# Kernel tuning notes

Measured on AMD Instinct MI355X. Metric: run time of the kernel, lower is better.

The kernel has to match this reference:

```python
import jax, jax.numpy as jnp
import numpy as np

T, D = 2048, 1024      # tokens, hidden_size
FF = 512               # moe_intermediate_size
E, K = 16, 4           # num_experts, top_k
L = 3                  # conv_L_cache (short causal conv width)
EPS = 1e-5
SCALE = 1.0            # routed_scaling_factor


def setup_inputs() -> dict:
    key = jax.random.key(0)
    ks = jax.random.split(key, 10)
    s = lambda k, shape, sc: jax.random.normal(k, shape, jnp.float32) * sc
    return {
        "hidden_states": s(ks[0], (T, D), 1.0),
        "residual": s(ks[1], (T, D), 1.0),
        "op_norm_w": jnp.ones((D,), jnp.float32),
        "ffn_norm_w": jnp.ones((D,), jnp.float32),
        "in_proj_w": s(ks[2], (3 * D, D), 0.02),   # produces B, C, x
        "conv_w": s(ks[3], (D, L), 0.2),            # depthwise causal kernel
        "out_proj_w": s(ks[4], (D, D), 0.02),
        "gate_w": s(ks[5], (E, D), 0.02),
        "gate_bias": s(ks[6], (E,), 0.1),           # e_score_correction_bias
        "w1": s(ks[7], (E, 2 * FF, D), 0.02),       # per-expert gate+up
        "w2": s(ks[8], (E, D, FF), 0.02),           # per-expert down
    }


def _fused_add_rmsnorm(x, w, res):
    # vLLM RMSNorm(x, residual): x += residual; residual = x; out = rmsnorm(x)*w
    x = x + res
    res = x
    v = jnp.mean(x * x, axis=-1, keepdims=True)
    return x * jax.lax.rsqrt(v + EPS) * w, res


def reference(hidden_states, residual, op_norm_w, ffn_norm_w, in_proj_w,
              conv_w, out_proj_w, gate_w, gate_bias, w1, w2):
    h, residual = _fused_add_rmsnorm(hidden_states, op_norm_w, residual)

    # ---- ShortConv mixer: Bx = B*x, causal depthwise conv, gate by C ----
    bcx = h @ in_proj_w.T                         # [T, 3D]
    B, C, x = jnp.split(bcx, 3, axis=-1)
    Bx = B * x
    xp = jnp.pad(Bx, ((L - 1, 0), (0, 0)))        # causal left-pad
    shifts = jnp.stack([xp[k:k + T] for k in range(L)], axis=0)  # [L,T,D]
    conv = jnp.einsum('ltd,dl->td', shifts, conv_w)
    y = (C * conv) @ out_proj_w.T                 # [T, D]

    h, residual = _fused_add_rmsnorm(y, ffn_norm_w, residual)

    # ---- Sparse MoE: sigmoid scoring + bias-corrected top-k, renormalize ----
    logits = h.astype(jnp.float32) @ gate_w.T     # [T, E]
    scores = jax.nn.sigmoid(logits)
    choice = scores + gate_bias                   # selection uses biased scores
    _, topi = jax.lax.top_k(choice, K)            # [T, K]
    w = jnp.take_along_axis(scores, topi, axis=-1)  # weights from raw scores
    w = w / (jnp.sum(w, axis=-1, keepdims=True) + 1e-20)  # norm_topk_prob
    cw = jnp.sum(jax.nn.one_hot(topi, E, dtype=h.dtype) * w[..., None].astype(h.dtype), axis=1)  # [T, E]

    # dense dispatch (reference): all experts on all tokens, masked combine
    gu = jnp.einsum('td,efd->etf', h, w1)         # [E, T, 2FF]
    g, u = jnp.split(gu, 2, axis=-1)
    act = jax.nn.silu(g) * u                      # SiluAndMul
    ye = jnp.einsum('etf,edf->etd', act, w2)      # [E, T, D]
    out = jnp.einsum('te,etd->td', cw, ye) * SCALE
    return out, residual
```

## Files before the change

kernel.cpp:

```cpp
#include <hip/hip_runtime.h>
#include <hip/hip_bf16.h>

#define T_  2048
#define D_  1024
#define FF_ 512
#define E_  16
#define K_  4
#define L_  3
static constexpr float EPS = 1e-5f;

typedef __hip_bfloat16 bf16;
typedef __attribute__((ext_vector_type(8))) short bf16x8;
typedef __attribute__((ext_vector_type(4))) float f32x4;

__device__ __forceinline__ float b2f(bf16 x) { return __bfloat162float(x); }

__device__ __forceinline__ unsigned int pk2(float a, float b) {
    __hip_bfloat162 h = __float22bfloat162_rn(make_float2(a, b));
    unsigned int u; __builtin_memcpy(&u, &h, 4); return u;
}

__device__ __forceinline__ void gload_lds16(const bf16* g, bf16* l) {
    __builtin_amdgcn_global_load_lds(
        (const __attribute__((address_space(1))) unsigned int*)g,
        (__attribute__((address_space(3))) unsigned int*)l, 16, 0, 0);
}

__device__ __forceinline__ void split_pack(float4 v, uint2 &hi, uint2 &lo) {
    __hip_bfloat162 h01 = __float22bfloat162_rn(make_float2(v.x, v.y));
    __hip_bfloat162 h23 = __float22bfloat162_rn(make_float2(v.z, v.w));
    float2 r01 = make_float2(v.x - __bfloat162float(h01.x), v.y - __bfloat162float(h01.y));
    float2 r23 = make_float2(v.z - __bfloat162float(h23.x), v.w - __bfloat162float(h23.y));
    __hip_bfloat162 l01 = __float22bfloat162_rn(r01);
    __hip_bfloat162 l23 = __float22bfloat162_rn(r23);
    __builtin_memcpy(&hi.x, &h01, 4); __builtin_memcpy(&hi.y, &h23, 4);
    __builtin_memcpy(&lo.x, &l01, 4); __builtin_memcpy(&lo.y, &l23, 4);
}

__global__ __launch_bounds__(256) void k_convert(const float* __restrict__ w1,
                                                 const float* __restrict__ w2,
                                                 const float* __restrict__ ipw,
                                                 const float* __restrict__ opw,
                                                 bf16* __restrict__ w1b,
                                                 bf16* __restrict__ w2b,
                                                 bf16* __restrict__ iph,
                                                 bf16* __restrict__ ipl,
                                                 bf16* __restrict__ oph,
                                                 bf16* __restrict__ opl) {
    const size_t n1 = (size_t)E_ * 2 * FF_ * D_;
    const size_t n2 = (size_t)E_ * D_ * FF_;
    const size_t n3 = (size_t)3 * D_ * D_;
    const size_t n4 = (size_t)D_ * D_;
    size_t i = ((size_t)blockIdx.x * 256 + threadIdx.x) * 8;
    if (i < n1) {
        float4 a = *(const float4*)&w1[i];
        float4 b = *(const float4*)&w1[i + 4];
        uint4 h; h.x = pk2(a.x, a.y); h.y = pk2(a.z, a.w);
        h.z = pk2(b.x, b.y); h.w = pk2(b.z, b.w);
        *(uint4*)&w1b[i] = h;
    } else if (i < n1 + n2) {
        size_t j = i - n1;
        float4 a = *(const float4*)&w2[j];
        float4 b = *(const float4*)&w2[j + 4];
        uint4 h; h.x = pk2(a.x, a.y); h.y = pk2(a.z, a.w);
        h.z = pk2(b.x, b.y); h.w = pk2(b.z, b.w);
        *(uint4*)&w2b[j] = h;
    } else if (i < n1 + n2 + n3) {
        size_t j = i - n1 - n2;
        float4 a = *(const float4*)&ipw[j];
        float4 b = *(const float4*)&ipw[j + 4];
        uint2 h0, l0, h1, l1;
        split_pack(a, h0, l0); split_pack(b, h1, l1);
        uint4 hh = make_uint4(h0.x, h0.y, h1.x, h1.y);
        uint4 ll = make_uint4(l0.x, l0.y, l1.x, l1.y);
        *(uint4*)&iph[j] = hh;
        *(uint4*)&ipl[j] = ll;
    } else if (i < n1 + n2 + n3 + n4) {
        size_t j = i - n1 - n2 - n3;
        float4 a = *(const float4*)&opw[j];
        float4 b = *(const float4*)&opw[j + 4];
        uint2 h0, l0, h1, l1;
        split_pack(a, h0, l0); split_pack(b, h1, l1);
        uint4 hh = make_uint4(h0.x, h0.y, h1.x, h1.y);
        uint4 ll = make_uint4(l0.x, l0.y, l1.x, l1.y);
        *(uint4*)&oph[j] = hh;
        *(uint4*)&opl[j] = ll;
    }
}

__device__ __forceinline__ float blockReduceSum(float v) {
    #pragma unroll
    for (int off = 32; off > 0; off >>= 1) v += __shfl_down(v, off, 64);
    __shared__ float s[4];
    __shared__ float tot;
    int lane = threadIdx.x & 63, wid = threadIdx.x >> 6;
    if (lane == 0) s[wid] = v;
    __syncthreads();
    if (threadIdx.x == 0) tot = s[0] + s[1] + s[2] + s[3];
    __syncthreads();
    return tot;
}

__global__ __launch_bounds__(256) void k_addnorm1z(const float* __restrict__ x,
                                                   const float* __restrict__ r,
                                                   const float* __restrict__ w,
                                                   bf16* __restrict__ hhi,
                                                   bf16* __restrict__ hlo,
                                                   float* __restrict__ res,
                                                   float* __restrict__ out0) {
    int t = blockIdx.x, tid = threadIdx.x;
    float v[4]; float ss = 0.f;
    #pragma unroll
    for (int i = 0; i < 4; i++) {
        int d = tid + 256 * i;
        float s = x[(size_t)t * D_ + d] + r[(size_t)t * D_ + d];
        v[i] = s; ss += s * s;
        out0[(size_t)t * D_ + d] = 0.f;
    }
    float tot = blockReduceSum(ss);
    float rs = rsqrtf(tot / (float)D_ + EPS);
    #pragma unroll
    for (int i = 0; i < 4; i++) {
        int d = tid + 256 * i;
        res[(size_t)t * D_ + d] = v[i];
        float val = v[i] * rs * w[d];
        bf16 hi = __float2bfloat16(val);
        hhi[(size_t)t * D_ + d] = hi;
        hlo[(size_t)t * D_ + d] = __float2bfloat16(val - b2f(hi));
    }
}

template<int TN>
__global__ __launch_bounds__(256) void k_gemm_small(const bf16* __restrict__ Ah,
                                                    const bf16* __restrict__ Al,
                                                    const bf16* __restrict__ Bh,
                                                    const bf16* __restrict__ Bl,
                                                    float* __restrict__ C,
                                                    int M, int N, int K) {
    constexpr int NF  = TN / 64;
    constexpr int NBG = TN / 32;
    __shared__ bf16 Ash[64 * 64];
    __shared__ bf16 Asl[64 * 64];
    __shared__ bf16 Bsh[TN * 64];
    __shared__ bf16 Bsl[TN * 64];
    int m0 = blockIdx.y * 64, n0 = blockIdx.x * TN;
    int tid = threadIdx.x;
    int wave = tid >> 6, lane = tid & 63, ml = lane & 15, quad = lane >> 4;
    int wn = wave * (TN / 4);
    int r0 = tid >> 3, q0 = tid & 7;
    const bf16 *sAh[2], *sAl[2];
    #pragma unroll
    for (int g = 0; g < 2; g++) {
        int ra = g * 32 + r0;
        int c = (q0 ^ (ra & 7)) << 3;
        sAh[g] = Ah + (size_t)(m0 + ra) * K + c;
        sAl[g] = Al + (size_t)(m0 + ra) * K + c;
    }
    const bf16 *sBh[NBG], *sBl[NBG];
    #pragma unroll
    for (int g = 0; g < NBG; g++) {
        int rb = g * 32 + r0;
        int c = (q0 ^ (rb & 7)) << 3;
        sBh[g] = Bh + (size_t)(n0 + rb) * K + c;
        sBl[g] = Bl + (size_t)(n0 + rb) * K + c;
    }
    int offA[2][4], offB[2][NF];
    #pragma unroll
    for (int ks = 0; ks < 2; ks++) {
        int cq = ks * 4 + quad;
        #pragma unroll
        for (int i = 0; i < 4; i++) {
            int ra = i * 16 + ml;
            offA[ks][i] = ra * 64 + ((cq ^ (ra & 7)) << 3);
        }
        #pragma unroll
        for (int j = 0; j < NF; j++) {
            int rb = wn + j * 16 + ml;
            offB[ks][j] = rb * 64 + ((cq ^ (rb & 7)) << 3);
        }
    }
    f32x4 acc[4][NF] = {};
    for (int kt = 0; kt < K; kt += 64) {
        #pragma unroll
        for (int g = 0; g < 2; g++) {
            gload_lds16(sAh[g] + kt, Ash + g * 2048 + wave * 512);
            gload_lds16(sAl[g] + kt, Asl + g * 2048 + wave * 512);
        }
        #pragma unroll
        for (int g = 0; g < NBG; g++) {
            gload_lds16(sBh[g] + kt, Bsh + g * 2048 + wave * 512);
            gload_lds16(sBl[g] + kt, Bsl + g * 2048 + wave * 512);
        }
        __syncthreads();
        #pragma unroll
        for (int ks = 0; ks < 2; ks++) {
            bf16x8 ah[4], al[4], bh[NF], bl[NF];
            #pragma unroll
            for (int i = 0; i < 4; i++) {
                ah[i] = *(const bf16x8*)&Ash[offA[ks][i]];
                al[i] = *(const bf16x8*)&Asl[offA[ks][i]];
            }
            #pragma unroll
            for (int j = 0; j < NF; j++) {
                bh[j] = *(const bf16x8*)&Bsh[offB[ks][j]];
                bl[j] = *(const bf16x8*)&Bsl[offB[ks][j]];
            }
            #pragma unroll
            for (int i = 0; i < 4; i++)
                #pragma unroll
                for (int j = 0; j < NF; j++) {
                    acc[i][j] = __builtin_amdgcn_mfma_f32_16x16x32_bf16(ah[i], bh[j], acc[i][j], 0, 0, 0);
                    acc[i][j] = __builtin_amdgcn_mfma_f32_16x16x32_bf16(al[i], bh[j], acc[i][j], 0, 0, 0);
                    acc[i][j] = __builtin_amdgcn_mfma_f32_16x16x32_bf16(ah[i], bl[j], acc[i][j], 0, 0, 0);
                }
        }
        __syncthreads();
    }
    #pragma unroll
    for (int i = 0; i < 4; i++)
        #pragma unroll
        for (int j = 0; j < NF; j++)
            #pragma unroll
            for (int r = 0; r < 4; r++) {
                int row = m0 + i * 16 + quad * 4 + r;
                int col = n0 + wn + j * 16 + ml;
                C[(size_t)row * N + col] = acc[i][j][r];
            }
}

__global__ __launch_bounds__(256) void k_gemm_split(const bf16* __restrict__ Ah,
                                                    const bf16* __restrict__ Al,
                                                    const float* __restrict__ B,
                                                    float* __restrict__ C,
                                                    int M, int N, int K) {
    __shared__ bf16 Ash[128][40];
    __shared__ bf16 Asl[128][40];
    __shared__ bf16 Bsh[128][40];
    __shared__ bf16 Bsl[128][40];
    int m0 = blockIdx.y * 128, n0 = blockIdx.x * 128;
    int tid = threadIdx.x;
    int wave = tid >> 6, lane = tid & 63, ml = lane & 15, quad = lane >> 4;
    int wm = (wave >> 1) * 64, wn = (wave & 1) * 64;
    f32x4 acc[4][4] = {};
    for (int kt = 0; kt < K; kt += 32) {
        #pragma unroll
        for (int p = 0; p < 2; p++) {
            int ch = p * 256 + tid, row = ch >> 2, c8 = (ch & 3) << 3;
            *(uint4*)&Ash[row][c8] = *(const uint4*)&Ah[(size_t)(m0 + row) * K + kt + c8];
            *(uint4*)&Asl[row][c8] = *(const uint4*)&Al[(size_t)(m0 + row) * K + kt + c8];
        }
        #pragma unroll
        for (int p = 0; p < 4; p++) {
            int ch = p * 256 + tid, row = ch >> 3, c4 = (ch & 7) << 2;
            float4 v = *(const float4*)&B[(size_t)(n0 + row) * K + kt + c4];
            uint2 hi, lo; split_pack(v, hi, lo);
            *(uint2*)&Bsh[row][c4] = hi;
            *(uint2*)&Bsl[row][c4] = lo;
        }
        __syncthreads();
        bf16x8 ah[4], al[4], bh[4], bl[4];
        #pragma unroll
        for (int i = 0; i < 4; i++) {
            ah[i] = *(const bf16x8*)&Ash[wm + i * 16 + ml][quad * 8];
            al[i] = *(const bf16x8*)&Asl[wm + i * 16 + ml][quad * 8];
        }
        #pragma unroll
        for (int j = 0; j < 4; j++) {
            bh[j] = *(const bf16x8*)&Bsh[wn + j * 16 + ml][quad * 8];
            bl[j] = *(const bf16x8*)&Bsl[wn + j * 16 + ml][quad * 8];
        }
        #pragma unroll
        for (int i = 0; i < 4; i++)
            #pragma unroll
            for (int j = 0; j < 4; j++) {
                acc[i][j] = __builtin_amdgcn_mfma_f32_16x16x32_bf16(ah[i], bh[j], acc[i][j], 0, 0, 0);
                acc[i][j] = __builtin_amdgcn_mfma_f32_16x16x32_bf16(al[i], bh[j], acc[i][j], 0, 0, 0);
                acc[i][j] = __builtin_amdgcn_mfma_f32_16x16x32_bf16(ah[i], bl[j], acc[i][j], 0, 0, 0);
            }
        __syncthreads();
    }
    #pragma unroll
    for (int i = 0; i < 4; i++)
        #pragma unroll
        for (int j = 0; j < 4; j++)
            #pragma unroll
            for (int r = 0; r < 4; r++) {
                int row = m0 + wm + i * 16 + quad * 4 + r;
                int col = n0 + wn + j * 16 + ml;
                C[(size_t)row * N + col] = acc[i][j][r];
            }
}

__global__ __launch_bounds__(256) void k_conv2(const float* __restrict__ bcx,
                                               const float* __restrict__ cw,
                                               bf16* __restrict__ cchi,
                                               bf16* __restrict__ cclo,
                                               int* __restrict__ zctl) {
    int t = blockIdx.x, tid = threadIdx.x;
    if (blockIdx.x == 0 && tid < 32) zctl[tid] = 0;
    #pragma unroll
    for (int i = 0; i < 4; i++) {
        int d = tid + 256 * i;
        float acc = 0.f;
        #pragma unroll
        for (int l = 0; l < L_; l++) {
            int tt = t + l - (L_ - 1);
            if (tt >= 0) {
                float bb = bcx[(size_t)tt * 3 * D_ + d];
                float xx = bcx[(size_t)tt * 3 * D_ + 2 * D_ + d];
                acc += bb * xx * cw[d * L_ + l];
            }
        }
        float c = bcx[(size_t)t * 3 * D_ + D_ + d];
        float val = c * acc;
        bf16 hi = __float2bfloat16(val);
        cchi[(size_t)t * D_ + d] = hi;
        cclo[(size_t)t * D_ + d] = __float2bfloat16(val - b2f(hi));
    }
}

__global__ __launch_bounds__(256) void k_an2_gate(const float* __restrict__ y,
                                                  float* __restrict__ res,
                                                  const float* __restrict__ w,
                                                  bf16* __restrict__ h2b,
                                                  const float* __restrict__ gw,
                                                  const float* __restrict__ gb,
                                                  int4* __restrict__ choice_idx,
                                                  float4* __restrict__ choice_wgt) {
    int t = blockIdx.x, tid = threadIdx.x;
    __shared__ float hs[D_];
    __shared__ float logits[E_];
    float v[4]; float ss = 0.f;
    #pragma unroll
    for (int i = 0; i < 4; i++) {
        int d = tid + 256 * i;
        float s = y[(size_t)t * D_ + d] + res[(size_t)t * D_ + d];
        v[i] = s; ss += s * s;
    }
    float tot = blockReduceSum(ss);
    float rs = rsqrtf(tot / (float)D_ + EPS);
    #pragma unroll
    for (int i = 0; i < 4; i++) {
        int d = tid + 256 * i;
        res[(size_t)t * D_ + d] = v[i];
        float val = v[i] * rs * w[d];
        h2b[(size_t)t * D_ + d] = __float2bfloat16(val);
        hs[d] = val;
    }
    __syncthreads();
    int e = tid >> 4, j = tid & 15;
    float p = 0.f;
    for (int d = j; d < D_; d += 16) p += hs[d] * gw[(size_t)e * D_ + d];
    #pragma unroll
    for (int off = 8; off > 0; off >>= 1) p += __shfl_down(p, off, 64);
    if (j == 0) logits[e] = p;
    __syncthreads();
    if (tid == 0) {
        float sc[E_], ch[E_];
        #pragma unroll
        for (int i = 0; i < E_; i++) {
            float s = 1.f / (1.f + expf(-logits[i]));
            sc[i] = s; ch[i] = s + gb[i];
        }
        int idx[K_]; float wv[K_]; float wsum = 0.f;
        bool used[E_] = {};
        #pragma unroll
        for (int k = 0; k < K_; k++) {
            int best = 0; float bv = -1e30f;
            for (int i = 0; i < E_; i++)
                if (!used[i] && ch[i] > bv) { bv = ch[i]; best = i; }
            used[best] = true; idx[k] = best; wv[k] = sc[best]; wsum += sc[best];
        }
        float inv = 1.f / (wsum + 1e-20f);
        choice_idx[t] = make_int4(idx[0], idx[1], idx[2], idx[3]);
        choice_wgt[t] = make_float4(wv[0] * inv, wv[1] * inv, wv[2] * inv, wv[3] * inv);
    }
}

__global__ __launch_bounds__(256) void k_scatter2(const int4* __restrict__ choice_idx,
                                                  const float4* __restrict__ choice_wgt,
                                                  int* __restrict__ cnt,
                                                  int* __restrict__ tok_list,
                                                  float* __restrict__ tok_w,
                                                  int* __restrict__ off,
                                                  int* __restrict__ done) {
    int e = blockIdx.x;
    __shared__ int ctr;
    if (threadIdx.x == 0) ctr = 0;
    __syncthreads();
    int lane = threadIdx.x & 63;
    for (int t = threadIdx.x; t < T_; t += 256) {
        int4   ci = choice_idx[t];
        float4 cw = choice_wgt[t];
        bool m = false; float w = 0.f;
        if (ci.x == e) { m = true; w = cw.x; }
        else if (ci.y == e) { m = true; w = cw.y; }
        else if (ci.z == e) { m = true; w = cw.z; }
        else if (ci.w == e) { m = true; w = cw.w; }
        unsigned long long mask = __ballot(m);
        int loff = __popcll(mask & ((1ull << lane) - 1ull));
        int wcnt = __popcll(mask);
        int base = 0;
        if (lane == 0 && wcnt > 0) base = atomicAdd(&ctr, wcnt);
        base = __shfl(base, 0, 64);
        if (m) {
            tok_list[e * T_ + base + loff] = t;
            tok_w[e * T_ + base + loff]    = w;
        }
    }
    __syncthreads();
    if (threadIdx.x == 0) {
        atomicExch(&cnt[e], ctr);
        __threadfence();
        int prev = atomicAdd(done, 1);
        if (prev == E_ - 1) {
            int s = 0;
            for (int i = 0; i < E_; i++) {
                int c = atomicAdd(&cnt[i], 0);
                off[i] = s; s += min(c, T_);
            }
            off[E_] = s;
        }
    }
}

__global__ __launch_bounds__(256) void k_moe_w1_pre(const bf16* __restrict__ h2,
                                                    const bf16* __restrict__ w1b,
                                                    const int* __restrict__ cnt,
                                                    const int* __restrict__ off,
                                                    const int* __restrict__ tok_list,
                                                    bf16* __restrict__ act) {
    int e = blockIdx.y >> 5, mt = blockIdx.y & 31;
    int m0 = mt * 64;
    int nt = min(cnt[e], T_);
    if (m0 >= nt) return;
    int n0 = blockIdx.x * 64;
    int base = off[e];
    __shared__ bf16 As[64 * 64];
    __shared__ bf16 Bg[64 * 64];
    __shared__ bf16 Bu[64 * 64];
    int tid = threadIdx.x;
    int wave = tid >> 6, lane = tid & 63, ml = lane & 15, quad = lane >> 4;
    const bf16* w1e = w1b + (size_t)e * 2 * FF_ * D_;
    int r0 = tid >> 3, q0 = tid & 7;
    int r1 = 32 + r0;
    int c0 = (q0 ^ (r0 & 7)) << 3;
    int c1 = (q0 ^ (r1 & 7)) << 3;
    int ma0 = m0 + r0, ma1 = m0 + r1;
    int tok0 = tok_list[e * T_ + (ma0 < nt ? ma0 : 0)] & (T_ - 1);
    int tok1 = tok_list[e * T_ + (ma1 < nt ? ma1 : 0)] & (T_ - 1);
    const bf16* sA0  = h2 + (size_t)tok0 * D_ + c0;
    const bf16* sA1  = h2 + (size_t)tok1 * D_ + c1;
    const bf16* sBg0 = w1e + (size_t)(n0 + r0) * D_ + c0;
    const bf16* sBg1 = w1e + (size_t)(n0 + r1) * D_ + c1;
    const bf16* sBu0 = w1e + (size_t)(FF_ + n0 + r0) * D_ + c0;
    const bf16* sBu1 = w1e + (size_t)(FF_ + n0 + r1) * D_ + c1;
    int dst0 = wave * 512, dst1 = 2048 + wave * 512;
    int offA[2], offB[2][4];
    #pragma unroll
    for (int ks = 0; ks < 2; ks++) {
        int ra = wave * 16 + ml;
        int cqa = ks * 4 + quad;
        offA[ks] = ra * 64 + ((cqa ^ (ra & 7)) << 3);
        #pragma unroll
        for (int j = 0; j < 4; j++) {
            int rb = j * 16 + ml;
            offB[ks][j] = rb * 64 + ((cqa ^ (rb & 7)) << 3);
        }
    }
    f32x4 ag[4] = {}, au[4] = {};
    for (int kt = 0; kt < D_; kt += 64) {
        gload_lds16(sA0 + kt,  As + dst0);
        gload_lds16(sA1 + kt,  As + dst1);
        gload_lds16(sBg0 + kt, Bg + dst0);
        gload_lds16(sBg1 + kt, Bg + dst1);
        gload_lds16(sBu0 + kt, Bu + dst0);
        gload_lds16(sBu1 + kt, Bu + dst1);
        __syncthreads();
        #pragma unroll
        for (int ks = 0; ks < 2; ks++) {
            bf16x8 a = *(const bf16x8*)&As[offA[ks]];
            #pragma unroll
            for (int j = 0; j < 4; j++) {
                bf16x8 bg = *(const bf16x8*)&Bg[offB[ks][j]];
                bf16x8 bu = *(const bf16x8*)&Bu[offB[ks][j]];
                ag[j] = __builtin_amdgcn_mfma_f32_16x16x32_bf16(a, bg, ag[j], 0, 0, 0);
                au[j] = __builtin_amdgcn_mfma_f32_16x16x32_bf16(a, bu, au[j], 0, 0, 0);
            }
        }
        __syncthreads();
    }
    #pragma unroll
    for (int j = 0; j < 4; j++)
        #pragma unroll
        for (int r = 0; r < 4; r++) {
            int m = m0 + wave * 16 + quad * 4 + r;
            if (m < nt) {
                float g = ag[j][r], u = au[j][r];
                float a = g / (1.f + __expf(-g)) * u;
                act[(size_t)(base + m) * FF_ + n0 + j * 16 + ml] = __float2bfloat16(a);
            }
        }
}

__global__ __launch_bounds__(256) void k_moe_w1(const bf16* __restrict__ h2,
                                                const float* __restrict__ w1,
                                                const int* __restrict__ cnt,
                                                const int* __restrict__ off,
                                                const int* __restrict__ tok_list,
                                                bf16* __restrict__ act) {
    int e = blockIdx.y >> 4, mt = blockIdx.y & 15;
    int m0 = mt * 128;
    int nt = min(cnt[e], T_);
    if (m0 >= nt) return;
    int n0 = blockIdx.x * 64;
    int base = off[e];
    __shared__ bf16 As[128][40];
    __shared__ bf16 Bg[64][40];
    __shared__ bf16 Bu[64][40];
    __shared__ int  toks[128];
    int tid = threadIdx.x;
    if (tid < 128) {
        int m = m0 + tid;
        toks[tid] = ((m < nt) ? tok_list[e * T_ + m] : tok_list[e * T_]) & (T_ - 1);
    }
    __syncthreads();
    const float* w1e = w1 + (size_t)e * 2 * FF_ * D_;
    int wave = tid >> 6, lane = tid & 63, ml = lane & 15, quad = lane >> 4;
    int wm = wave * 32;
    f32x4 ag[2][4] = {}, au[2][4] = {};
    for (int kt = 0; kt < D_; kt += 32) {
        #pragma unroll
        for (int p = 0; p < 2; p++) {
            int ch = p * 256 + tid, row = ch >> 2, c8 = (ch & 3) << 3;
            *(uint4*)&As[row][c8] = *(const uint4*)&h2[(size_t)toks[row] * D_ + kt + c8];
        }
        #pragma unroll
        for (int p = 0; p < 2; p++) {
            int ch = p * 256 + tid, row = ch >> 3, c4 = (ch & 7) << 2;
            float4 vg = *(const float4*)&w1e[(size_t)(n0 + row) * D_ + kt + c4];
            float4 vu = *(const float4*)&w1e[(size_t)(FF_ + n0 + row) * D_ + kt + c4];
            uint2 wg; wg.x = pk2(vg.x, vg.y); wg.y = pk2(vg.z, vg.w);
            uint2 wu; wu.x = pk2(vu.x, vu.y); wu.y = pk2(vu.z, vu.w);
            *(uint2*)&Bg[row][c4] = wg;
            *(uint2*)&Bu[row][c4] = wu;
        }
        __syncthreads();
        bf16x8 a[2], bg[4], bu[4];
        #pragma unroll
        for (int i = 0; i < 2; i++) a[i] = *(const bf16x8*)&As[wm + i * 16 + ml][quad * 8];
        #pragma unroll
        for (int j = 0; j < 4; j++) {
            bg[j] = *(const bf16x8*)&Bg[j * 16 + ml][quad * 8];
            bu[j] = *(const bf16x8*)&Bu[j * 16 + ml][quad * 8];
        }
        #pragma unroll
        for (int i = 0; i < 2; i++)
            #pragma unroll
            for (int j = 0; j < 4; j++) {
                ag[i][j] = __builtin_amdgcn_mfma_f32_16x16x32_bf16(a[i], bg[j], ag[i][j], 0, 0, 0);
                au[i][j] = __builtin_amdgcn_mfma_f32_16x16x32_bf16(a[i], bu[j], au[i][j], 0, 0, 0);
            }
        __syncthreads();
    }
    #pragma unroll
    for (int i = 0; i < 2; i++)
        #pragma unroll
        for (int j = 0; j < 4; j++)
            #pragma unroll
            for (int r = 0; r < 4; r++) {
                int m = m0 + wm + i * 16 + quad * 4 + r;
                if (m < nt) {
                    float g = ag[i][j][r], u = au[i][j][r];
                    float a = g / (1.f + __expf(-g)) * u;
                    act[(size_t)(base + m) * FF_ + n0 + j * 16 + ml] = __float2bfloat16(a);
                }
            }
}

__global__ __launch_bounds__(256) void k_moe_w2_pre(const bf16* __restrict__ act,
                                                    const bf16* __restrict__ w2b,
                                                    const int* __restrict__ cnt,
                                                    const int* __restrict__ off,
                                                    const int* __restrict__ tok_list,
                                                    const float* __restrict__ tok_w,
                                                    float* __restrict__ out0) {
    int e = blockIdx.y >> 5, mt = blockIdx.y & 31;
    int m0 = mt * 64;
    int nt = min(cnt[e], T_);
    if (m0 >= nt) return;
    int n0 = blockIdx.x * 128;
    int base = off[e];
    __shared__ bf16 As[64 * 64];
    __shared__ bf16 Bs[128 * 64];
    int tid = threadIdx.x;
    int wave = tid >> 6, lane = tid & 63, ml = lane & 15, quad = lane >> 4;
    int wm = (wave >> 1) * 32, wn = (wave & 1) * 64;
    const bf16* w2e = w2b + (size_t)e * D_ * FF_;
    int r0 = tid >> 3, q0 = tid & 7;
    int ra1 = 32 + r0;
    int ca0 = (q0 ^ (r0 & 7)) << 3;
    int ca1 = (q0 ^ (ra1 & 7)) << 3;
    const bf16* sA0 = act + (size_t)(base + m0 + r0)  * FF_ + ca0;
    const bf16* sA1 = act + (size_t)(base + m0 + ra1) * FF_ + ca1;
    const bf16* sB[4];
    #pragma unroll
    for (int g = 0; g < 4; g++) {
        int rb = g * 32 + r0;
        int cb = (q0 ^ (rb & 7)) << 3;
        sB[g] = w2e + (size_t)(n0 + rb) * FF_ + cb;
    }
    int dstA0 = wave * 512, dstA1 = 2048 + wave * 512;
    int offA[2][2], offB[2][4];
    #pragma unroll
    for (int ks = 0; ks < 2; ks++) {
        int cq = ks * 4 + quad;
        #pragma unroll
        for (int i = 0; i < 2; i++) {
            int ra = wm + i * 16 + ml;
            offA[ks][i] = ra * 64 + ((cq ^ (ra & 7)) << 3);
        }
        #pragma unroll
        for (int j = 0; j < 4; j++) {
            int rb = wn + j * 16 + ml;
            offB[ks][j] = rb * 64 + ((cq ^ (rb & 7)) << 3);
        }
    }
    f32x4 acc[2][4] = {};
    for (int kt = 0; kt < FF_; kt += 64) {
        gload_lds16(sA0 + kt, As + dstA0);
        gload_lds16(sA1 + kt, As + dstA1);
        #pragma unroll
        for (int g = 0; g < 4; g++)
            gload_lds16(sB[g] + kt, Bs + g * 2048 + wave * 512);
        __syncthreads();
        #pragma unroll
        for (int ks = 0; ks < 2; ks++) {
            bf16x8 a[2], b[4];
            #pragma unroll
            for (int i = 0; i < 2; i++) a[i] = *(const bf16x8*)&As[offA[ks][i]];
            #pragma unroll
            for (int j = 0; j < 4; j++) b[j] = *(const bf16x8*)&Bs[offB[ks][j]];
            #pragma unroll
            for (int i = 0; i < 2; i++)
                #pragma unroll
                for (int j = 0; j < 4; j++)
                    acc[i][j] = __builtin_amdgcn_mfma_f32_16x16x32_bf16(a[i], b[j], acc[i][j], 0, 0, 0);
        }
        __syncthreads();
    }
    #pragma unroll
    for (int i = 0; i < 2; i++)
        #pragma unroll
        for (int r = 0; r < 4; r++) {
            int m = m0 + wm + i * 16 + quad * 4 + r;
            if (m < nt) {
                int   tok = tok_list[e * T_ + m] & (T_ - 1);
                float wgt = tok_w[e * T_ + m];
                #pragma unroll
                for (int j = 0; j < 4; j++) {
                    int col = n0 + wn + j * 16 + ml;
                    atomicAdd(&out0[(size_t)tok * D_ + col], wgt * acc[i][j][r]);
                }
            }
        }
}

__global__ __launch_bounds__(256) void k_moe_w2(const bf16* __restrict__ act,
                                                const float* __restrict__ w2,
                                                const int* __restrict__ cnt,
                                                const int* __restrict__ off,
                                                const int* __restrict__ tok_list,
                                                const float* __restrict__ tok_w,
                                                float* __restrict__ out0) {
    int e = blockIdx.y >> 4, mt = blockIdx.y & 15;
    int m0 = mt * 128;
    int nt = min(cnt[e], T_);
    if (m0 >= nt) return;
    int n0 = blockIdx.x * 128;
    int base = off[e];
    __shared__ bf16 As[128][40];
    __shared__ bf16 Bs[128][40];
    int tid = threadIdx.x;
    int wave = tid >> 6, lane = tid & 63, ml = lane & 15, quad = lane >> 4;
    int wm = (wave >> 1) * 64, wn = (wave & 1) * 64;
    const float* w2e = w2 + (size_t)e * D_ * FF_;
    f32x4 acc[4][4] = {};
    for (int kt = 0; kt < FF_; kt += 32) {
        #pragma unroll
        for (int p = 0; p < 2; p++) {
            int ch = p * 256 + tid, row = ch >> 2, c8 = (ch & 3) << 3;
            uint4 v = make_uint4(0, 0, 0, 0);
            if (m0 + row < nt) v = *(const uint4*)&act[(size_t)(base + m0 + row) * FF_ + kt + c8];
            *(uint4*)&As[row][c8] = v;
        }
        #pragma unroll
        for (int p = 0; p < 4; p++) {
            int ch = p * 256 + tid, row = ch >> 3, c4 = (ch & 7) << 2;
            float4 v = *(const float4*)&w2e[(size_t)(n0 + row) * FF_ + kt + c4];
            uint2 w; w.x = pk2(v.x, v.y); w.y = pk2(v.z, v.w);
            *(uint2*)&Bs[row][c4] = w;
        }
        __syncthreads();
        bf16x8 a[4], b[4];
        #pragma unroll
        for (int i = 0; i < 4; i++) a[i] = *(const bf16x8*)&As[wm + i * 16 + ml][quad * 8];
        #pragma unroll
        for (int j = 0; j < 4; j++) b[j] = *(const bf16x8*)&Bs[wn + j * 16 + ml][quad * 8];
        #pragma unroll
        for (int i = 0; i < 4; i++)
            #pragma unroll
            for (int j = 0; j < 4; j++)
                acc[i][j] = __builtin_amdgcn_mfma_f32_16x16x32_bf16(a[i], b[j], acc[i][j], 0, 0, 0);
        __syncthreads();
    }
    #pragma unroll
    for (int i = 0; i < 4; i++)
        #pragma unroll
        for (int r = 0; r < 4; r++) {
            int m = m0 + wm + i * 16 + quad * 4 + r;
            if (m < nt) {
                int   tok = tok_list[e * T_ + m] & (T_ - 1);
                float wgt = tok_w[e * T_ + m];
                #pragma unroll
                for (int j = 0; j < 4; j++) {
                    int col = n0 + wn + j * 16 + ml;
                    atomicAdd(&out0[(size_t)tok * D_ + col], wgt * acc[i][j][r]);
                }
            }
        }
}

extern "C" void kernel_launch(void* const* d_in, const int* in_sizes, int n_in,
                              void* d_out, int out_size, void* d_ws, size_t ws_size,
                              hipStream_t stream) {
    const float* hidden     = (const float*)d_in[0];
    const float* residual   = (const float*)d_in[1];
    const float* op_norm_w  = (const float*)d_in[2];
    const float* ffn_norm_w = (const float*)d_in[3];
    const float* in_proj_w  = (const float*)d_in[4];
    const float* conv_w     = (const float*)d_in[5];
    const float* out_proj_w = (const float*)d_in[6];
    const float* gate_w     = (const float*)d_in[7];
    const float* gate_bias  = (const float*)d_in[8];
    const float* w1         = (const float*)d_in[9];
    const float* w2         = (const float*)d_in[10];

    char* p = (char*)d_ws;
    int*    cnt        = (int*)p;        p += 256;
    int*    off        = (int*)p;        p += 128;
    int*    tok_list   = (int*)p;        p += (size_t)E_ * T_ * 4;
    float*  tok_w      = (float*)p;      p += (size_t)E_ * T_ * 4;
    int4*   choice_idx = (int4*)p;       p += (size_t)T_ * 16;
    float4* choice_wgt = (float4*)p;     p += (size_t)T_ * 16;
    char*   regA       = p;              p += (size_t)T_ * D_ * 2 * 2;
    char*   regB       = p;              p += (size_t)T_ * 3 * D_ * 4;

    const size_t n1 = (size_t)E_ * 2 * FF_ * D_;
    const size_t n2 = (size_t)E_ * D_ * FF_;
    const size_t n3 = (size_t)3 * D_ * D_;
    const size_t n4 = (size_t)D_ * D_;
    bf16* w1b = (bf16*)p;  p += n1 * 2;
    bf16* w2b = (bf16*)p;  p += n2 * 2;
    bf16* iph = (bf16*)p;  p += n3 * 2;
    bf16* ipl = (bf16*)p;  p += n3 * 2;
    bf16* oph = (bf16*)p;  p += n4 * 2;
    bf16* opl = (bf16*)p;  p += n4 * 2;
    bool pre = ((size_t)(p - (char*)d_ws) <= ws_size);

    bf16* h1hi = (bf16*)regA;
    bf16* h1lo = (bf16*)(regA + (size_t)T_ * D_ * 2);
    bf16* cchi = h1hi;
    bf16* cclo = h1lo;
    bf16* act  = (bf16*)regA;
    float* bcx = (float*)regB;
    float* y   = (float*)regB;
    bf16*  h2b = (bf16*)(regB + (size_t)T_ * D_ * 8);

    float* out0 = (float*)d_out;
    float* res  = out0 + (size_t)T_ * D_;

    if (pre) {
        int nq = (int)((n1 + n2 + n3 + n4) / 8 / 256);
        k_convert<<<nq, 256, 0, stream>>>(w1, w2, in_proj_w, out_proj_w,
                                          w1b, w2b, iph, ipl, oph, opl);
    }
    k_addnorm1z<<<T_, 256, 0, stream>>>(hidden, residual, op_norm_w, h1hi, h1lo, res, out0);
    if (pre)
        k_gemm_small<128><<<dim3(3 * D_ / 128, T_ / 64), 256, 0, stream>>>(
            h1hi, h1lo, iph, ipl, bcx, T_, 3 * D_, D_);
    else
        k_gemm_split<<<dim3(3 * D_ / 128, T_ / 128), 256, 0, stream>>>(
            h1hi, h1lo, in_proj_w, bcx, T_, 3 * D_, D_);
    k_conv2<<<T_, 256, 0, stream>>>(bcx, conv_w, cchi, cclo, cnt);
    if (pre)
        k_gemm_small<64><<<dim3(D_ / 64, T_ / 64), 256, 0, stream>>>(
            cchi, cclo, oph, opl, y, T_, D_, D_);
    else
        k_gemm_split<<<dim3(D_ / 128, T_ / 128), 256, 0, stream>>>(
            cchi, cclo, out_proj_w, y, T_, D_, D_);
    k_an2_gate<<<T_, 256, 0, stream>>>(y, res, ffn_norm_w, h2b, gate_w, gate_bias,
                                       choice_idx, choice_wgt);
    k_scatter2<<<E_, 256, 0, stream>>>(choice_idx, choice_wgt, cnt, tok_list, tok_w,
                                       off, &cnt[31]);
    if (pre) {
        k_moe_w1_pre<<<dim3(FF_ / 64, E_ * (T_ / 64)), 256, 0, stream>>>(
            h2b, w1b, cnt, off, tok_list, act);
        k_moe_w2_pre<<<dim3(D_ / 128, E_ * (T_ / 64)), 256, 0, stream>>>(
            act, w2b, cnt, off, tok_list, tok_w, out0);
    } else {
        k_moe_w1<<<dim3(FF_ / 64, E_ * (T_ / 128)), 256, 0, stream>>>(
            h2b, w1, cnt, off, tok_list, act);
        k_moe_w2<<<dim3(D_ / 128, E_ * (T_ / 128)), 256, 0, stream>>>(
            act, w2, cnt, off, tok_list, tok_w, out0);
    }
}
```

Before: 361.6 us.

## Replace MoE down-proj atomic scatter with per-slot buffer and gather combine

The expert down-projection now writes weighted per-slot outputs into a compact bf16 buffer instead of atomically adding into the output. The scatter kernel records each token's slot position per expert. A new per-token combine kernel then sums the four expert contributions. This removes fp32 global atomics, at the cost of an extra kernel launch, an extra buffer round trip and bf16 rounding of partials.

```diff
diff --git a/kernel.cpp b/kernel.cpp
--- a/kernel.cpp
+++ b/kernel.cpp
@@ -382,6 +382,7 @@
                                                   int* __restrict__ cnt,
                                                   int* __restrict__ tok_list,
                                                   float* __restrict__ tok_w,
+                                                  int* __restrict__ pos4,
                                                   int* __restrict__ off,
                                                   int* __restrict__ done) {
     int e = blockIdx.x;
@@ -392,11 +393,12 @@
     for (int t = threadIdx.x; t < T_; t += 256) {
         int4   ci = choice_idx[t];
         float4 cw = choice_wgt[t];
-        bool m = false; float w = 0.f;
-        if (ci.x == e) { m = true; w = cw.x; }
-        else if (ci.y == e) { m = true; w = cw.y; }
-        else if (ci.z == e) { m = true; w = cw.z; }
-        else if (ci.w == e) { m = true; w = cw.w; }
+        int kidx = -1; float w = 0.f;
+        if (ci.x == e)      { kidx = 0; w = cw.x; }
+        else if (ci.y == e) { kidx = 1; w = cw.y; }
+        else if (ci.z == e) { kidx = 2; w = cw.z; }
+        else if (ci.w == e) { kidx = 3; w = cw.w; }
+        bool m = (kidx >= 0);
         unsigned long long mask = __ballot(m);
         int loff = __popcll(mask & ((1ull << lane) - 1ull));
         int wcnt = __popcll(mask);
@@ -406,6 +408,7 @@
         if (m) {
             tok_list[e * T_ + base + loff] = t;
             tok_w[e * T_ + base + loff]    = w;
+            pos4[t * 4 + kidx]             = base + loff;
         }
     }
     __syncthreads();
@@ -582,9 +585,8 @@
                                                     const bf16* __restrict__ w2b,
                                                     const int* __restrict__ cnt,
                                                     const int* __restrict__ off,
-                                                    const int* __restrict__ tok_list,
                                                     const float* __restrict__ tok_w,
-                                                    float* __restrict__ out0) {
+                                                    bf16* __restrict__ ye) {
     int e = blockIdx.y >> 5, mt = blockIdx.y & 31;
     int m0 = mt * 64;
     int nt = min(cnt[e], T_);
@@ -655,15 +657,34 @@
         for (int r = 0; r < 4; r++) {
             int m = m0 + wm + i * 16 + quad * 4 + r;
             if (m < nt) {
-                int   tok = tok_list[e * T_ + m] & (T_ - 1);
                 float wgt = tok_w[e * T_ + m];
                 #pragma unroll
                 for (int j = 0; j < 4; j++) {
                     int col = n0 + wn + j * 16 + ml;
-                    atomicAdd(&out0[(size_t)tok * D_ + col], wgt * acc[i][j][r]);
+                    ye[(size_t)(base + m) * D_ + col] = __float2bfloat16(wgt * acc[i][j][r]);
                 }
             }
         }
+}
+
+__global__ __launch_bounds__(256) void k_combine(const bf16* __restrict__ ye,
+                                                 const int4* __restrict__ choice_idx,
+                                                 const int4* __restrict__ pos4,
+                                                 const int* __restrict__ off,
+                                                 float* __restrict__ out0) {
+    int t = blockIdx.x, tid = threadIdx.x;
+    int4 ci = choice_idx[t];
+    int4 ps = pos4[t];
+    size_t rr0 = (size_t)(off[ci.x] + ps.x) * D_;
+    size_t rr1 = (size_t)(off[ci.y] + ps.y) * D_;
+    size_t rr2 = (size_t)(off[ci.z] + ps.z) * D_;
+    size_t rr3 = (size_t)(off[ci.w] + ps.w) * D_;
+    #pragma unroll
+    for (int i = 0; i < 4; i++) {
+        int d = tid + 256 * i;
+        out0[(size_t)t * D_ + d] = b2f(ye[rr0 + d]) + b2f(ye[rr1 + d])
+                                 + b2f(ye[rr2 + d]) + b2f(ye[rr3 + d]);
+    }
 }
 
 __global__ __launch_bounds__(256) void k_moe_w2(const bf16* __restrict__ act,
@@ -753,6 +774,7 @@
     float*  tok_w      = (float*)p;      p += (size_t)E_ * T_ * 4;
     int4*   choice_idx = (int4*)p;       p += (size_t)T_ * 16;
     float4* choice_wgt = (float4*)p;     p += (size_t)T_ * 16;
+    int4*   pos4       = (int4*)p;       p += (size_t)T_ * 16;
     char*   regA       = p;              p += (size_t)T_ * D_ * 2 * 2;
     char*   regB       = p;              p += (size_t)T_ * 3 * D_ * 4;
 
@@ -775,6 +797,7 @@
     bf16* act  = (bf16*)regA;
     float* bcx = (float*)regB;
     float* y   = (float*)regB;
+    bf16*  ye  = (bf16*)regB;
     bf16*  h2b = (bf16*)(regB + (size_t)T_ * D_ * 8);
 
     float* out0 = (float*)d_out;
@@ -802,12 +825,13 @@
     k_an2_gate<<<T_, 256, 0, stream>>>(y, res, ffn_norm_w, h2b, gate_w, gate_bias,
                                        choice_idx, choice_wgt);
     k_scatter2<<<E_, 256, 0, stream>>>(choice_idx, choice_wgt, cnt, tok_list, tok_w,
-                                       off, &cnt[31]);
+                                       (int*)pos4, off, &cnt[31]);
     if (pre) {
         k_moe_w1_pre<<<dim3(FF_ / 64, E_ * (T_ / 64)), 256, 0, stream>>>(
             h2b, w1b, cnt, off, tok_list, act);
         k_moe_w2_pre<<<dim3(D_ / 128, E_ * (T_ / 64)), 256, 0, stream>>>(
-            act, w2b, cnt, off, tok_list, tok_w, out0);
+            act, w2b, cnt, off, tok_w, ye);
+        k_combine<<<T_, 256, 0, stream>>>(ye, choice_idx, pos4, off, out0);
     } else {
         k_moe_w1<<<dim3(FF_ / 64, E_ * (T_ / 128)), 256, 0, stream>>>(
             h2b, w1, cnt, off, tok_list, act);
```

After: 355.5 us. Within noise of the previous version (-1.7%).
